# Kernel tuning notes

Hardware: AMD Instinct MI355X
Metric: run time of the kernel (lower is better)

The kernel has to match this reference:

```python
import jax, jax.numpy as jnp
import numpy as np

NUM_HEADS = 12


def _get_rel_pos(q_size, k_size, rel_pos):
    # q_size == k_size here, so the torch interpolate branch is never taken;
    # table already has 2*max(q,k)-1 rows. Gather by relative coordinate.
    coords = jnp.arange(q_size)[:, None] - jnp.arange(k_size)[None, :] + (k_size - 1)
    return rel_pos[coords]  # (q_size, k_size, head_dim)


def setup_inputs() -> dict:
    key = jax.random.key(0)
    ks = jax.random.split(key, 8)
    B, D, H, W, dim = 32, 8, 8, 8, 768
    hd = dim // NUM_HEADS
    s = 0.02
    return {
        "x": jax.random.normal(ks[0], (B, D, H, W, dim), jnp.float32),
        "w_qkv": jax.random.normal(ks[1], (dim, 3 * dim), jnp.float32) * s,
        "b_qkv": jnp.zeros((3 * dim,), jnp.float32),
        "w_proj": jax.random.normal(ks[2], (dim, dim), jnp.float32) * s,
        "b_proj": jnp.zeros((dim,), jnp.float32),
        "rel_pos_d": jax.random.normal(ks[3], (2 * D - 1, hd), jnp.float32) * s,
        "rel_pos_h": jax.random.normal(ks[4], (2 * H - 1, hd), jnp.float32) * s,
        "rel_pos_w": jax.random.normal(ks[5], (2 * W - 1, hd), jnp.float32) * s,
    }


def reference(x, w_qkv, b_qkv, w_proj, b_proj, rel_pos_d, rel_pos_h, rel_pos_w):
    B, D, H, W, dim = x.shape
    nH = NUM_HEADS
    hd = dim // nH
    N = D * H * W
    scale = hd ** -0.5

    # qkv projection: (B, N, 3, nH, hd) -> (3, B*nH, N, hd)
    qkv = (x.reshape(B, N, dim) @ w_qkv + b_qkv).reshape(B, N, 3, nH, hd)
    qkv = jnp.transpose(qkv, (2, 0, 3, 1, 4)).reshape(3, B * nH, N, hd)
    q, k, v = qkv[0], qkv[1], qkv[2]

    attn = jnp.einsum('bqc,bkc->bqk', q * scale, k)  # (B*nH, N, N)

    # decomposed relative positional bias (MViTv2-style)
    Rd = _get_rel_pos(D, D, rel_pos_d)  # (D, D, hd)
    Rh = _get_rel_pos(H, H, rel_pos_h)  # (H, H, hd)
    Rw = _get_rel_pos(W, W, rel_pos_w)  # (W, W, hd)
    r_q = q.reshape(B * nH, D, H, W, hd)
    rel_d = jnp.einsum('bdhwc,dkc->bdhwk', r_q, Rd)
    rel_h = jnp.einsum('bdhwc,hkc->bdhwk', r_q, Rh)
    rel_w = jnp.einsum('bdhwc,wkc->bdhwk', r_q, Rw)

    attn = attn.reshape(B * nH, D, H, W, D, H, W)
    attn = (attn
            + rel_d[:, :, :, :, :, None, None]
            + rel_h[:, :, :, :, None, :, None]
            + rel_w[:, :, :, :, None, None, :])
    attn = jax.nn.softmax(attn.reshape(B * nH, N, N), axis=-1)

    out = (attn @ v).reshape(B, nH, D, H, W, hd)
    out = jnp.transpose(out, (0, 2, 3, 4, 1, 5)).reshape(B, D, H, W, dim)
    return out @ w_proj + b_proj
```

## Files before the change

kernel.cpp:

```cpp
#include <hip/hip_runtime.h>
#include <hip/hip_bf16.h>
#include <cstdint>

typedef __bf16 bf16x8 __attribute__((ext_vector_type(8)));
typedef __bf16 bf16x4 __attribute__((ext_vector_type(4)));
typedef float  f32x4  __attribute__((ext_vector_type(4)));
typedef float  f32x16 __attribute__((ext_vector_type(16)));
typedef unsigned u32x4 __attribute__((ext_vector_type(4)));

__device__ __forceinline__ f32x4 mfma16(bf16x8 a, bf16x8 b, f32x4 c) {
  return __builtin_amdgcn_mfma_f32_16x16x32_bf16(a, b, c, 0, 0, 0);
}
__device__ __forceinline__ f32x16 mfma32(bf16x8 a, bf16x8 b, f32x16 c) {
  return __builtin_amdgcn_mfma_f32_32x32x16_bf16(a, b, c, 0, 0, 0);
}

__device__ __forceinline__ void gload_lds16(const __bf16* g, __bf16* l) {
  __builtin_amdgcn_global_load_lds(
      (const __attribute__((address_space(1))) void*)g,
      (__attribute__((address_space(3))) void*)l, 16, 0, 0);
}

__device__ __forceinline__ unsigned cvtpk(float lo, float hi) {
  unsigned r;
  asm("v_cvt_pk_bf16_f32 %0, %1, %2" : "=v"(r) : "v"(lo), "v"(hi));
  return r;
}
__device__ __forceinline__ void plswap(unsigned& a, unsigned& b) {
  asm("v_permlane32_swap_b32 %0, %1" : "+v"(a), "+v"(b));
}

__global__ __launch_bounds__(256) void cvt_bf16_kernel(const float* __restrict__ in,
                                                       __bf16* __restrict__ out, int n4) {
  int i = blockIdx.x * 256 + threadIdx.x;
  if (i < n4) {
    float4 v = ((const float4*)in)[i];
    bf16x4 o;
    o[0] = (__bf16)v.x; o[1] = (__bf16)v.y; o[2] = (__bf16)v.z; o[3] = (__bf16)v.w;
    ((bf16x4*)out)[i] = o;
  }
}

__global__ __launch_bounds__(256) void transpose_cvt_kernel(const float* __restrict__ src,
                                                            __bf16* __restrict__ dst,
                                                            int R, int C) {
  __shared__ float tile[32][33];
  int r0 = blockIdx.y * 32, c0 = blockIdx.x * 32;
  int tx = threadIdx.x & 31, ty = threadIdx.x >> 5;
#pragma unroll
  for (int i = 0; i < 4; ++i)
    tile[ty + i * 8][tx] = src[(size_t)(r0 + ty + i * 8) * C + c0 + tx];
  __syncthreads();
#pragma unroll
  for (int i = 0; i < 4; ++i) {
    int rr = ty + i * 8;
    dst[(size_t)(c0 + rr) * R + r0 + tx] = (__bf16)tile[tx][rr];
  }
}

template <int EPI>
__global__ __launch_bounds__(512) void gemm_bt3_kernel(
    const __bf16* __restrict__ A, const __bf16* __restrict__ Bt,
    int M, int N, int K, int nbx,
    const float* __restrict__ bias,
    float* __restrict__ outF,
    __bf16* __restrict__ qo, __bf16* __restrict__ ko, __bf16* __restrict__ vTo) {
  __shared__ __attribute__((aligned(16))) __bf16 lA[3][256 * 64];
  __shared__ __attribute__((aligned(16))) __bf16 lB[3][128 * 64];
  const int t = threadIdx.x;
  const int l = t & 63, w = t >> 6;
  const int wm = (w >> 1) * 64, wn = (w & 1) * 64;
  const int cpx = gridDim.x >> 3;
  const int wg = (blockIdx.x & 7) * cpx + (blockIdx.x >> 3);
  const int m0 = (wg / nbx) * 256, n0 = (wg % nbx) * 128;
  const int nk = K >> 6;

  auto stage = [&](int buf, int kt, int part) {
    const __bf16* As = A + (size_t)m0 * K + kt * 64;
    const __bf16* Bs = Bt + (size_t)n0 * K + kt * 64;
#pragma unroll
    for (int r2 = 0; r2 < 2; ++r2) {
      int li = (part * 2 + r2) * 512 + t;
      int row = li >> 3, pc = li & 7, lc = pc ^ (row & 7);
      gload_lds16(As + (size_t)row * K + lc * 8, &lA[buf][li * 8]);
    }
    {
      int li = part * 512 + t;
      int row = li >> 3, pc = li & 7, lc = pc ^ (row & 7);
      gload_lds16(Bs + (size_t)row * K + lc * 8, &lB[buf][li * 8]);
    }
  };

  f32x4 acc[4][4] = {};
  stage(0, 0, 0); stage(0, 0, 1);
  stage(1, 1, 0); stage(1, 1, 1);

  for (int j = 0; j < nk; ++j) {
    asm volatile("s_waitcnt vmcnt(6)" ::: "memory");
    __builtin_amdgcn_s_barrier();
    __builtin_amdgcn_sched_barrier(0);
    const __bf16* la = &lA[j % 3][0];
    const __bf16* lb = &lB[j % 3][0];
    const int st = (j + 2 < nk) ? j + 2 : j;
    const int sb = (j + 2) % 3;
#pragma unroll
    for (int p = 0; p < 2; ++p) {
      bf16x8 af[4], bfv[4];
#pragma unroll
      for (int mt = 0; mt < 4; ++mt) {
        int row = wm + mt * 16 + (l & 15);
        int ch = (p * 4 + (l >> 4)) ^ (row & 7);
        af[mt] = *(const bf16x8*)(la + row * 64 + ch * 8);
      }
#pragma unroll
      for (int nt = 0; nt < 4; ++nt) {
        int row = wn + nt * 16 + (l & 15);
        int ch = (p * 4 + (l >> 4)) ^ (row & 7);
        bfv[nt] = *(const bf16x8*)(lb + row * 64 + ch * 8);
      }
      stage(sb, st, p);
      __builtin_amdgcn_s_setprio(1);
#pragma unroll
      for (int mt = 0; mt < 4; ++mt)
#pragma unroll
        for (int nt = 0; nt < 4; ++nt)
          acc[mt][nt] = mfma16(af[mt], bfv[nt], acc[mt][nt]);
      __builtin_amdgcn_s_setprio(0);
    }
  }

#pragma unroll
  for (int mt = 0; mt < 4; ++mt) {
#pragma unroll
    for (int nt = 0; nt < 4; ++nt) {
#pragma unroll
      for (int r = 0; r < 4; ++r) {
        int row = m0 + wm + mt * 16 + (l >> 4) * 4 + r;
        int col = n0 + wn + nt * 16 + (l & 15);
        float val = acc[mt][nt][r] + bias[col];
        if constexpr (EPI == 0) {
          int s = col / 768, rem = col - s * 768;
          int h = rem >> 6, c = rem & 63;
          int b = row >> 9, n = row & 511;
          size_t bh = (size_t)(b * 12 + h);
          __bf16 bv = (__bf16)val;
          if (s == 0)      qo[(bh * 512 + n) * 64 + c] = bv;
          else if (s == 1) ko[(bh * 512 + n) * 64 + c] = bv;
          else             vTo[(bh * 64 + c) * 512 + n] = bv;
        } else {
          outF[(size_t)row * N + col] = val;
        }
      }
    }
  }
}

__device__ __forceinline__ const bf16x8* kfrag(const __bf16* base, int row, int ch) {
  return (const bf16x8*)(base + row * 64 + ((ch ^ (row & 7)) * 8));
}
__device__ __forceinline__ const bf16x8* vfrag(const __bf16* base, int row, int ch) {
  return (const bf16x8*)(base + row * 32 + ((ch ^ ((row >> 1) & 3)) * 8));
}

__global__ __launch_bounds__(256, 4) void attn_kernel(
    const __bf16* __restrict__ qg_, const __bf16* __restrict__ kg,
    const __bf16* __restrict__ vT,
    const float* __restrict__ rpd, const float* __restrict__ rph,
    const float* __restrict__ rpw,
    __bf16* __restrict__ attn_out) {
  const int bid = (blockIdx.x & 7) * 192 + (blockIdx.x >> 3);
  const int bh = bid >> 2;
  const int qb = bid & 3;
  const int t = threadIdx.x, w = t >> 6, l = t & 63;
  const int lq = l & 31, lh5 = l >> 5;

  __shared__ float bias_lds[128][25];
  __shared__ float rs_lds[4][32];
  __shared__ __attribute__((aligned(16))) __bf16 k_lds[2][32 * 64];
  __shared__ __attribute__((aligned(16))) __bf16 v_lds[2][64 * 32];

  const __bf16* kb = kg + (size_t)bh * 512 * 64;
  const __bf16* vb = vT + (size_t)bh * 64 * 512;

  auto stage = [&](int sbuf, int j0) {
    {
      int row = t >> 3, pc = t & 7;
      int lc = pc ^ (row & 7);
      gload_lds16(kb + (size_t)(j0 + row) * 64 + lc * 8, &k_lds[sbuf][t * 8]);
    }
    {
      int row = t >> 2, pc = t & 3;
      int lc = pc ^ ((row >> 1) & 3);
      gload_lds16(vb + (size_t)row * 512 + j0 + lc * 8, &v_lds[sbuf][t * 8]);
    }
  };

  stage(0, 0);

  const __bf16* qbase = qg_ + ((size_t)bh * 512 + qb * 128 + w * 32) * 64;
  bf16x8 qf[4];
#pragma unroll
  for (int s = 0; s < 4; ++s)
    qf[s] = *(const bf16x8*)(qbase + lq * 64 + s * 16 + lh5 * 8);

  {
    const int row = w * 32 + lq;
    const int n = qb * 128 + row;
    const int dd = n >> 6, hh = (n >> 3) & 7, ww = n & 7;
#pragma unroll
    for (int jt = 0; jt < 2; ++jt) {
      const float* src;
      if (jt == 0) src = (lq < 15) ? rpd + (size_t)lq * 64
                                   : (lq >= 16 && lq < 31) ? rph + (size_t)(lq - 16) * 64
                                                           : nullptr;
      else         src = (lq < 15) ? rpw + (size_t)lq * 64 : nullptr;
      f32x16 cb = {};
#pragma unroll
      for (int s = 0; s < 4; ++s) {
        bf16x8 afr;
        if (src) {
          float4 a = *(const float4*)(src + s * 16 + lh5 * 8);
          float4 b = *(const float4*)(src + s * 16 + lh5 * 8 + 4);
          u32x4 u = {cvtpk(a.x, a.y), cvtpk(a.z, a.w), cvtpk(b.x, b.y), cvtpk(b.z, b.w)};
          afr = __builtin_bit_cast(bf16x8, u);
        } else {
          afr = bf16x8{};
        }
        cb = mfma32(afr, qf[s], cb);
      }
#pragma unroll
      for (int r = 0; r < 16; ++r) {
        int j = (r & 3) + 8 * (r >> 2) + 4 * lh5;
        if (jt == 0) {
          if (j < 16) {
            int idx = dd + 7 - j;
            if (idx >= 0 && idx < 8) bias_lds[row][idx] = cb[r];
          } else {
            int idx = hh + 7 - (j - 16);
            if (idx >= 0 && idx < 8) bias_lds[row][8 + idx] = cb[r];
          }
        } else {
          if (j < 16) {
            int idx = ww + 7 - j;
            if (idx >= 0 && idx < 8) bias_lds[row][16 + idx] = cb[r];
          }
        }
      }
    }
  }

  __syncthreads();

  const float LOG2E = 1.44269504f;
  const float* brow = &bias_lds[w * 32 + lq][0];
  float bh2e[4], bh2o[4], bw2[4];
#pragma unroll
  for (int rr = 0; rr < 4; ++rr) {
    bh2e[rr] = brow[8 + rr] * LOG2E;
    bh2o[rr] = brow[12 + rr] * LOG2E;
    bw2[rr] = brow[16 + rr + 4 * lh5] * LOG2E;
  }

  f32x16 accO0 = {}, accO1 = {};
  float rs4[4] = {0.f, 0.f, 0.f, 0.f};
  const float scale2 = 0.125f * LOG2E;

  for (int kk = 0; kk < 8; ++kk) {
#pragma unroll
    for (int par = 0; par < 2; ++par) {
      const int kb_i = kk * 2 + par;
      if (kb_i < 15) stage(par ^ 1, (kb_i + 1) * 32);
      const __bf16* kl = k_lds[par];
      const __bf16* vl = v_lds[par];

      f32x16 accS = {};
#pragma unroll
      for (int s = 0; s < 4; ++s)
        accS = mfma32(*kfrag(kl, lq, lh5 + 2 * s), qf[s], accS);

      float bd2 = brow[kb_i >> 1] * LOG2E;
      float pr[16];
#pragma unroll
      for (int rr = 0; rr < 4; ++rr) {
        float bsum = bd2 + (par ? bh2o[rr] : bh2e[rr]);
#pragma unroll
        for (int c = 0; c < 4; ++c) {
          int r = rr * 4 + c;
          float p = __builtin_amdgcn_exp2f(accS[r] * scale2 + bsum + bw2[c]);
          rs4[rr] += p;
          pr[r] = p;
        }
      }

      unsigned a0 = cvtpk(pr[0], pr[1]),   b0 = cvtpk(pr[4], pr[5]);
      unsigned a1 = cvtpk(pr[2], pr[3]),   b1 = cvtpk(pr[6], pr[7]);
      unsigned a2 = cvtpk(pr[8], pr[9]),   b2 = cvtpk(pr[12], pr[13]);
      unsigned a3 = cvtpk(pr[10], pr[11]), b3 = cvtpk(pr[14], pr[15]);
      plswap(a0, b0); plswap(a1, b1); plswap(a2, b2); plswap(a3, b3);
      u32x4 u0 = {a0, a1, b0, b1};
      u32x4 u1 = {a2, a3, b2, b3};
      bf16x8 pf0 = __builtin_bit_cast(bf16x8, u0);
      bf16x8 pf1 = __builtin_bit_cast(bf16x8, u1);

      accO0 = mfma32(pf0, *vfrag(vl, lq, lh5), accO0);
      accO0 = mfma32(pf1, *vfrag(vl, lq, lh5 + 2), accO0);
      accO1 = mfma32(pf0, *vfrag(vl, 32 + lq, lh5), accO1);
      accO1 = mfma32(pf1, *vfrag(vl, 32 + lq, lh5 + 2), accO1);

      __syncthreads();
    }
  }

  {
    float rsum = (rs4[0] + rs4[1]) + (rs4[2] + rs4[3]);
    float s = rsum + __shfl_xor(rsum, 32);
    if (l < 32) rs_lds[w][l] = 1.f / s;
  }

  const int b_ = bh / 12, h_ = bh - b_ * 12;
  __bf16* obase = attn_out + ((size_t)b_ * 512 + qb * 128 + w * 32) * 768 + h_ * 64;
#pragma unroll
  for (int rr = 0; rr < 4; ++rr) {
#pragma unroll
    for (int c = 0; c < 4; ++c) {
      int r = rr * 4 + c;
      int qrow = c + 8 * rr + 4 * lh5;
      float inv = rs_lds[w][qrow];
      obase[(size_t)qrow * 768 + lq]      = (__bf16)(accO0[r] * inv);
      obase[(size_t)qrow * 768 + 32 + lq] = (__bf16)(accO1[r] * inv);
    }
  }
}

extern "C" void kernel_launch(void* const* d_in, const int* in_sizes, int n_in,
                              void* d_out, int out_size, void* d_ws, size_t ws_size,
                              hipStream_t stream) {
  const float* x      = (const float*)d_in[0];
  const float* w_qkv  = (const float*)d_in[1];
  const float* b_qkv  = (const float*)d_in[2];
  const float* w_proj = (const float*)d_in[3];
  const float* b_proj = (const float*)d_in[4];
  const float* rpd    = (const float*)d_in[5];
  const float* rph    = (const float*)d_in[6];
  const float* rpw    = (const float*)d_in[7];
  float* out = (float*)d_out;

  char* base = (char*)d_ws;
  __bf16* xb     = (__bf16*)(base);
  __bf16* wqkvT  = (__bf16*)(base + 25165824);
  __bf16* wprojT = (__bf16*)(base + 25165824 + 3538944);
  __bf16* qb     = (__bf16*)(base + 25165824 + 3538944 + 1179648);
  __bf16* kb     = qb + (size_t)384 * 512 * 64;
  __bf16* vT     = kb + (size_t)384 * 512 * 64;

  cvt_bf16_kernel<<<12288, 256, 0, stream>>>(x, xb, 12582912 / 4);
  transpose_cvt_kernel<<<dim3(2304 / 32, 768 / 32), 256, 0, stream>>>(w_qkv, wqkvT, 768, 2304);
  transpose_cvt_kernel<<<dim3(768 / 32, 768 / 32), 256, 0, stream>>>(w_proj, wprojT, 768, 768);

  gemm_bt3_kernel<0><<<1152, 512, 0, stream>>>(
      xb, wqkvT, 16384, 2304, 768, 18, b_qkv, nullptr, qb, kb, vT);

  attn_kernel<<<1536, 256, 0, stream>>>(qb, kb, vT, rpd, rph, rpw, xb);

  gemm_bt3_kernel<1><<<384, 512, 0, stream>>>(
      xb, wprojT, 16384, 768, 768, 6, b_proj, out, nullptr, nullptr, nullptr);
}
```

Baseline: 189.2 us.

## Triple-buffer K/V staging in attention and vectorize QKV epilogue stores

The attention loop moves from double to triple buffering of K/V tiles in LDS. Each iteration now does one explicit vmcnt wait plus a barrier, then issues the prefetch two tiles ahead after the QK^T MFMAs, replacing the trailing __syncthreads. This gives global-to-LDS loads more time to land and removes one barrier from the critical path. It also raises MFMA priority around the PV product. Separately, the QKV GEMM epilogue now computes the index once per 4-row fragment, writes V^T as a packed bf16x4 store and uses strided stores for Q/K. The cost is about 8 KB more LDS per block, which could reduce occupancy.

```diff
diff --git a/kernel.cpp b/kernel.cpp
--- a/kernel.cpp
+++ b/kernel.cpp
@@ -133,23 +133,27 @@
   for (int mt = 0; mt < 4; ++mt) {
 #pragma unroll
     for (int nt = 0; nt < 4; ++nt) {
-#pragma unroll
-      for (int r = 0; r < 4; ++r) {
-        int row = m0 + wm + mt * 16 + (l >> 4) * 4 + r;
-        int col = n0 + wn + nt * 16 + (l & 15);
-        float val = acc[mt][nt][r] + bias[col];
-        if constexpr (EPI == 0) {
-          int s = col / 768, rem = col - s * 768;
-          int h = rem >> 6, c = rem & 63;
-          int b = row >> 9, n = row & 511;
-          size_t bh = (size_t)(b * 12 + h);
-          __bf16 bv = (__bf16)val;
-          if (s == 0)      qo[(bh * 512 + n) * 64 + c] = bv;
-          else if (s == 1) ko[(bh * 512 + n) * 64 + c] = bv;
-          else             vTo[(bh * 64 + c) * 512 + n] = bv;
+      int col = n0 + wn + nt * 16 + (l & 15);
+      int row0 = m0 + wm + mt * 16 + (l >> 4) * 4;
+      if constexpr (EPI == 0) {
+        int s = col / 768, rem = col - s * 768;
+        int h = rem >> 6, c = rem & 63;
+        int b = row0 >> 9, n = row0 & 511;
+        size_t bh = (size_t)(b * 12 + h);
+        if (s == 2) {
+          bf16x4 pv;
+#pragma unroll
+          for (int r = 0; r < 4; ++r) pv[r] = (__bf16)(acc[mt][nt][r] + bias[col]);
+          *(bf16x4*)(vTo + (bh * 64 + c) * 512 + n) = pv;
         } else {
-          outF[(size_t)row * N + col] = val;
+          __bf16* dst = (s == 0 ? qo : ko) + (bh * 512 + n) * 64 + c;
+#pragma unroll
+          for (int r = 0; r < 4; ++r) dst[(size_t)r * 64] = (__bf16)(acc[mt][nt][r] + bias[col]);
         }
+      } else {
+#pragma unroll
+        for (int r = 0; r < 4; ++r)
+          outF[(size_t)(row0 + r) * N + col] = acc[mt][nt][r] + bias[col];
       }
     }
   }
@@ -176,8 +180,8 @@
 
   __shared__ float bias_lds[128][25];
   __shared__ float rs_lds[4][32];
-  __shared__ __attribute__((aligned(16))) __bf16 k_lds[2][32 * 64];
-  __shared__ __attribute__((aligned(16))) __bf16 v_lds[2][64 * 32];
+  __shared__ __attribute__((aligned(16))) __bf16 k_lds[3][32 * 64];
+  __shared__ __attribute__((aligned(16))) __bf16 v_lds[3][64 * 32];
 
   const __bf16* kb = kg + (size_t)bh * 512 * 64;
   const __bf16* vb = vT + (size_t)bh * 64 * 512;
@@ -196,6 +200,7 @@
   };
 
   stage(0, 0);
+  stage(1, 32);
 
   const __bf16* qbase = qg_ + ((size_t)bh * 512 + qb * 128 + w * 32) * 64;
   bf16x8 qf[4];
@@ -269,14 +274,20 @@
 #pragma unroll
     for (int par = 0; par < 2; ++par) {
       const int kb_i = kk * 2 + par;
-      if (kb_i < 15) stage(par ^ 1, (kb_i + 1) * 32);
-      const __bf16* kl = k_lds[par];
-      const __bf16* vl = v_lds[par];
+      asm volatile("s_waitcnt vmcnt(2)" ::: "memory");
+      __builtin_amdgcn_s_barrier();
+      __builtin_amdgcn_sched_barrier(0);
+      const __bf16* kl = k_lds[kb_i % 3];
+      const __bf16* vl = v_lds[kb_i % 3];
+      const int st = (kb_i + 2 < 16) ? kb_i + 2 : kb_i;
+      const int sb = (kb_i + 2) % 3;
 
       f32x16 accS = {};
 #pragma unroll
       for (int s = 0; s < 4; ++s)
         accS = mfma32(*kfrag(kl, lq, lh5 + 2 * s), qf[s], accS);
+
+      stage(sb, st * 32);
 
       float bd2 = brow[kb_i >> 1] * LOG2E;
       float pr[16];
@@ -302,12 +313,12 @@
       bf16x8 pf0 = __builtin_bit_cast(bf16x8, u0);
       bf16x8 pf1 = __builtin_bit_cast(bf16x8, u1);
 
+      __builtin_amdgcn_s_setprio(1);
       accO0 = mfma32(pf0, *vfrag(vl, lq, lh5), accO0);
       accO0 = mfma32(pf1, *vfrag(vl, lq, lh5 + 2), accO0);
       accO1 = mfma32(pf0, *vfrag(vl, 32 + lq, lh5), accO1);
       accO1 = mfma32(pf1, *vfrag(vl, 32 + lq, lh5 + 2), accO1);
-
-      __syncthreads();
+      __builtin_amdgcn_s_setprio(0);
     }
   }
 
```

Result: faster. 172.6 us (median of 2 runs) (-8.8%).
